# Kernel tuning notes

Hardware: AMD Instinct MI355X
Metric: run time of the kernel (lower is better)

The kernel has to match this reference:

```python
import jax, jax.numpy as jnp
import numpy as np

N_QUBITS = 14
N_TROTTER = 10
EVO_TIME = 1.0
BATCH = 2048
DIM = 2 ** N_QUBITS

# (-1)**bit_q(idx) for every basis index (Qiskit little-endian: qubit q <-> bit q)
_bits = (np.arange(DIM)[:, None] >> np.arange(N_QUBITS)[None, :]) & 1
_SIGNS = np.asarray(1 - 2 * _bits, dtype=np.float32)  # (DIM, n)


def _apply_1q(psi, U, q, n):
    A = 2 ** (n - 1 - q)
    B = 2 ** q
    psi = psi.reshape(A, 2, B)
    psi = jnp.einsum('ij,ajb->aib', U, psi)
    return psi.reshape(-1)


def _apply_zz(psi, theta, q, n):
    # CX(q,q+1); RZ(theta) on q+1; CX(q,q+1)  ==  diagonal exp(-i*theta/2 * Z_q Z_{q+1})
    A = 2 ** (n - 2 - q)
    B = 2 ** q
    em = jnp.exp(-0.5j * theta)
    ep = jnp.exp(0.5j * theta)
    diag = jnp.stack([em, ep, ep, em])  # axis index = 2*bit_{q+1} + bit_q
    psi = psi.reshape(A, 4, B) * diag[None, :, None]
    return psi.reshape(-1)


def _base_state(J, g):
    # Fixed part of the circuit (same for every sample): H on all qubits, then Trotter steps.
    n = N_QUBITS
    dt = EVO_TIME / N_TROTTER
    inv = 1.0 / np.sqrt(2.0)
    H = jnp.array([[inv, inv], [inv, -inv]], dtype=jnp.complex64)
    psi = jnp.zeros(DIM, dtype=jnp.complex64).at[0].set(1.0)
    for q in range(n):
        psi = _apply_1q(psi, H, q, n)
    for _ in range(N_TROTTER):
        for i in range(n - 1):
            psi = _apply_zz(psi, J[i] * dt, i, n)
        for i in range(n):
            half = 0.5 * g[i] * dt
            c = jnp.cos(half).astype(jnp.complex64)
            ms = -1j * jnp.sin(half)
            RX = jnp.stack([jnp.stack([c, ms]), jnp.stack([ms, c])])
            psi = _apply_1q(psi, RX, i, n)
    return psi


def _expectations(psi):
    # psi: (batch, DIM). Original observable order: block i -> qubit n-1-i, [X, Y, Z].
    n = N_QUBITS
    outs = []
    for i in range(n):
        q = n - 1 - i
        A = 2 ** (n - 1 - q)
        B = 2 ** q
        pr = psi.reshape(-1, A, 2, B)
        p0 = pr[:, :, 0, :]
        p1 = pr[:, :, 1, :]
        c = jnp.sum(jnp.conj(p0) * p1, axis=(1, 2))
        outs.append(2.0 * jnp.real(c))  # <X_q>
        outs.append(2.0 * jnp.imag(c))  # <Y_q>
        outs.append(jnp.sum(p0.real ** 2 + p0.imag ** 2 - p1.real ** 2 - p1.imag ** 2, axis=(1, 2)))  # <Z_q>
    return jnp.stack(outs, axis=1).astype(jnp.float32)


def setup_inputs() -> dict:
    key = jax.random.key(0)
    kx, kj, kg = jax.random.split(key, 3)
    x = jax.random.normal(kx, (BATCH, N_QUBITS), dtype=jnp.float32)
    J = jax.random.uniform(kj, (N_QUBITS - 1,), minval=0.5, maxval=1.5, dtype=jnp.float32)
    g = jax.random.uniform(kg, (N_QUBITS,), minval=0.5, maxval=1.5, dtype=jnp.float32)
    return {"x": x, "J": J, "g": g}


def reference(x, J, g):
    psi0 = _base_state(J, g)  # (DIM,), shared across the batch
    S = jnp.asarray(_SIGNS)   # (DIM, n)
    # Final per-sample RZ(x[b,q]) on qubit q -> diagonal phase exp(-i/2 * sum_q x_q * (-1)^bit_q)
    phase = jnp.exp((-0.5j) * (x @ S.T).astype(jnp.complex64))  # (batch, DIM)
    psi = psi0[None, :] * phase
    return _expectations(psi)
```

## Files before the change

kernel.cpp:

```cpp
#include <hip/hip_runtime.h>

#define NQ     14
#define DIMQ   16384
#define NTROT  10
#define NWG    16
#define NTHR   256

typedef float vfloat4 __attribute__((ext_vector_type(4)));

struct Smem {
    float2 slab[1024];
    float2 tabLo[64];
    float2 tabHi[128];
    float  red[48];
};

__device__ __forceinline__ float2 d2f2(double d) { union { double d; float2 f; } u; u.d = d; return u.f; }
__device__ __forceinline__ double f22d(float2 f) { union { double d; float2 f; } u; u.f = f; return u.d; }

__device__ __forceinline__ void ld4c(const float2* p, float2 r[4]) {
    vfloat4 a, b;
    asm volatile("global_load_dwordx4 %0, %2, off sc0 sc1\n\t"
                 "global_load_dwordx4 %1, %2, off offset:16 sc0 sc1\n\t"
                 "s_waitcnt vmcnt(0)"
                 : "=&v"(a), "=&v"(b) : "v"(p) : "memory");
    r[0] = make_float2(a.x, a.y); r[1] = make_float2(a.z, a.w);
    r[2] = make_float2(b.x, b.y); r[3] = make_float2(b.z, b.w);
}
__device__ __forceinline__ void st4c(float2* p, const float2 r[4]) {
    vfloat4 a, b;
    a.x = r[0].x; a.y = r[0].y; a.z = r[1].x; a.w = r[1].y;
    b.x = r[2].x; b.y = r[2].y; b.z = r[3].x; b.w = r[3].y;
    asm volatile("global_store_dwordx4 %0, %1, off sc0 sc1\n\t"
                 "global_store_dwordx4 %0, %2, off offset:16 sc0 sc1"
                 : : "v"(p), "v"(a), "v"(b) : "memory");
}
__device__ __forceinline__ void st2(float2* p, float2 v) {
    asm volatile("global_store_dwordx2 %0, %1, off sc0 sc1"
                 : : "v"(p), "v"(f22d(v)) : "memory");
}
__device__ __forceinline__ void stf(float* p, float v) {
    asm volatile("global_store_dword %0, %1, off sc0 sc1" : : "v"(p), "v"(v) : "memory");
}
__device__ __forceinline__ float ldf(const float* p) {
    float v;
    asm volatile("global_load_dword %0, %1, off sc0 sc1\n\ts_waitcnt vmcnt(0)"
                 : "=&v"(v) : "v"(p) : "memory");
    return v;
}
__device__ __forceinline__ void sti(int* p, int v) {
    asm volatile("global_store_dword %0, %1, off sc0 sc1" : : "v"(p), "v"(v) : "memory");
}
__device__ __forceinline__ int ldi(const int* p) {
    int v;
    asm volatile("global_load_dword %0, %1, off sc0 sc1\n\ts_waitcnt vmcnt(0)"
                 : "=&v"(v) : "v"(p) : "memory");
    return v;
}

__device__ __forceinline__ void gbar(int* flags, int w, int phase) {
    asm volatile("s_waitcnt vmcnt(0)" ::: "memory");
    __syncthreads();
    if (threadIdx.x < 64) {
        if (threadIdx.x == 0) sti(&flags[w], phase);
        for (;;) {
            int v = phase;
            if (threadIdx.x < NWG) v = ldi(&flags[threadIdx.x]);
            if (__ballot(v >= phase) == ~0ull) break;
            __builtin_amdgcn_s_sleep(1);
        }
    }
    __syncthreads();
}

__device__ __forceinline__ float2 cmulf(float2 a, float2 b) {
    return make_float2(a.x * b.x - a.y * b.y, a.x * b.y + a.y * b.x);
}
__device__ __forceinline__ void bfly(float2& p0, float2& p1, float c, float s) {
    float2 n0 = make_float2(c * p0.x + s * p1.y, c * p0.y - s * p1.x);
    float2 n1 = make_float2(c * p1.x + s * p0.y, c * p1.y - s * p0.x);
    p0 = n0; p1 = n1;
}
__device__ __forceinline__ void bfly_shfl(float2& p, int mask, float c, float s) {
    float qx = __shfl_xor(p.x, mask);
    float qy = __shfl_xor(p.y, mask);
    p = make_float2(c * p.x + s * qy, c * p.y - s * qx);
}
__device__ __forceinline__ void zz_apply(const Smem& sm, float2& a, int k) {
    int d = (k ^ (k >> 1)) & 0x1FFF;
    float2 rot = cmulf(sm.tabLo[d & 63], sm.tabHi[d >> 6]);
    a = cmulf(a, rot);
}
__device__ __forceinline__ void stage_12(float2* slab, float2 r[4], int t) {
    __syncthreads();
#pragma unroll
    for (int j = 0; j < 4; ++j) slab[(t << 2) | j] = r[j];
    __syncthreads();
#pragma unroll
    for (int j = 0; j < 4; ++j) r[j] = slab[t | (j << 8)];
}
__device__ __forceinline__ void stage_21(float2* slab, float2 r[4], int t) {
    __syncthreads();
#pragma unroll
    for (int j = 0; j < 4; ++j) slab[t | (j << 8)] = r[j];
    __syncthreads();
#pragma unroll
    for (int j = 0; j < 4; ++j) r[j] = slab[(t << 2) | j];
}
__device__ __forceinline__ void reduce_qubit(Smem& sm, int sb, int i, int t) {
    float cr = 0.f, ci = 0.f, z = 0.f;
#pragma unroll
    for (int j = 0; j < 4; ++j) {
        const int m = (t << 2) | j;
        const float2 a = sm.slab[m];
        const float n = a.x * a.x + a.y * a.y;
        if ((m >> sb) & 1) {
            z -= n;
        } else {
            z += n;
            const float2 b = sm.slab[m ^ (1 << sb)];
            cr += a.x * b.x + a.y * b.y;
            ci += a.x * b.y - a.y * b.x;
        }
    }
#pragma unroll
    for (int off = 32; off; off >>= 1) {
        cr += __shfl_down(cr, off);
        ci += __shfl_down(ci, off);
        z  += __shfl_down(z, off);
    }
    if ((t & 63) == 0) {
        atomicAdd(&sm.red[3 * i + 0], cr);
        atomicAdd(&sm.red[3 * i + 1], ci);
        atomicAdd(&sm.red[3 * i + 2], z);
    }
}

template <bool FIRST>
__device__ void phaseA(Smem& sm, float2* psi, int w, int t,
                       const float* c, const float* s) {
    float2 r[4];
    if (FIRST) {
#pragma unroll
        for (int j = 0; j < 4; ++j) r[j] = make_float2(0.0078125f, 0.0f);
    } else {
        ld4c(&psi[(w << 10) | (t << 2)], r);
#pragma unroll
        for (int b = 2; b < 6; ++b) {
#pragma unroll
            for (int j = 0; j < 4; ++j) bfly_shfl(r[j], 1 << b, c[2 + b], s[2 + b]);
        }
    }
#pragma unroll
    for (int j = 0; j < 4; ++j) zz_apply(sm, r[j], (w << 10) | (t << 2) | j);
    bfly(r[0], r[1], c[0], s[0]); bfly(r[2], r[3], c[0], s[0]);
    bfly(r[0], r[2], c[1], s[1]); bfly(r[1], r[3], c[1], s[1]);
#pragma unroll
    for (int b = 0; b < 6; ++b) {
#pragma unroll
        for (int j = 0; j < 4; ++j) bfly_shfl(r[j], 1 << b, c[2 + b], s[2 + b]);
    }
    stage_12(sm.slab, r, t);
    bfly(r[0], r[1], c[8], s[8]); bfly(r[2], r[3], c[8], s[8]);
    bfly(r[0], r[2], c[9], s[9]); bfly(r[1], r[3], c[9], s[9]);
#pragma unroll
    for (int j = 0; j < 4; ++j) st2(&psi[(w << 10) | t | (j << 8)], r[j]);
}

template <bool REDUCE>
__device__ void phaseB(Smem& sm, float2* psi, int w, int t,
                       const float* c, const float* s) {
    float2 r[4];
    const int kbase = ((t >> 2) << 8) | (w << 4) | ((t & 3) << 2);
    ld4c(&psi[kbase], r);
#pragma unroll
    for (int j = 0; j < 4; ++j) bfly_shfl(r[j], 16, c[10], s[10]);
#pragma unroll
    for (int j = 0; j < 4; ++j) bfly_shfl(r[j], 32, c[11], s[11]);
    stage_12(sm.slab, r, t);
    bfly(r[0], r[1], c[12], s[12]); bfly(r[2], r[3], c[12], s[12]);
    bfly(r[0], r[2], c[13], s[13]); bfly(r[1], r[3], c[13], s[13]);
#pragma unroll
    for (int j = 0; j < 4; ++j) {
        const int m = t | (j << 8);
        zz_apply(sm, r[j], ((m >> 4) << 8) | (w << 4) | (m & 15));
    }
    bfly(r[0], r[1], c[12], s[12]); bfly(r[2], r[3], c[12], s[12]);
    bfly(r[0], r[2], c[13], s[13]); bfly(r[1], r[3], c[13], s[13]);
#pragma unroll
    for (int b = 0; b < 4; ++b) {
#pragma unroll
        for (int j = 0; j < 4; ++j) bfly_shfl(r[j], 1 << b, c[b], s[b]);
    }
#pragma unroll
    for (int j = 0; j < 4; ++j) bfly_shfl(r[j], 16, c[8], s[8]);
#pragma unroll
    for (int j = 0; j < 4; ++j) bfly_shfl(r[j], 32, c[9], s[9]);
    stage_21(sm.slab, r, t);
#pragma unroll
    for (int j = 0; j < 4; ++j) bfly_shfl(r[j], 16, c[10], s[10]);
#pragma unroll
    for (int j = 0; j < 4; ++j) bfly_shfl(r[j], 32, c[11], s[11]);
    st4c(&psi[kbase], r);

    if (REDUCE) {
#pragma unroll
        for (int j = 0; j < 4; ++j) sm.slab[(t << 2) | j] = r[j];
        __syncthreads();
#pragma unroll
        for (int q = 0; q <= 3; ++q) reduce_qubit(sm, q, 13 - q, t);
#pragma unroll
        for (int q = 8; q <= 13; ++q) reduce_qubit(sm, q - 4, 13 - q, t);
    }
}

__device__ void phaseA_final(Smem& sm, const float2* psi, int w, int t,
                             const float* c, const float* s, float* P) {
    float2 r[4];
    ld4c(&psi[(w << 10) | (t << 2)], r);
#pragma unroll
    for (int b = 2; b < 6; ++b) {
#pragma unroll
        for (int j = 0; j < 4; ++j) bfly_shfl(r[j], 1 << b, c[2 + b], s[2 + b]);
    }
    __syncthreads();
#pragma unroll
    for (int j = 0; j < 4; ++j) sm.slab[(t << 2) | j] = r[j];
    __syncthreads();
#pragma unroll
    for (int q = 4; q <= 7; ++q) reduce_qubit(sm, q, 13 - q, t);
    __syncthreads();
    if (t < 42) stf(&P[t * NWG + w], sm.red[t]);
}

extern "C" __global__ void __launch_bounds__(NTHR)
qr_all(const float* __restrict__ x, const float* __restrict__ J,
       const float* __restrict__ g, float* __restrict__ out,
       float2* __restrict__ psi, float* __restrict__ P,
       int* __restrict__ flags) {
    __shared__ Smem sm;
    const int w = blockIdx.x;
    const int t = threadIdx.x;
    const float dt = 0.1f;

    if (t < 64) {
        float phi = 0.0f;
        for (int i = 0; i < 6; ++i) {
            const float h = 0.5f * J[i] * dt;
            phi += ((t >> i) & 1) ? h : -h;
        }
        float sn, cs; __sincosf(phi, &sn, &cs);
        sm.tabLo[t] = make_float2(cs, sn);
    } else if (t < 192) {
        const int v = t - 64;
        float phi = 0.0f;
        for (int i = 0; i < 7; ++i) {
            const float h = 0.5f * J[6 + i] * dt;
            phi += ((v >> i) & 1) ? h : -h;
        }
        float sn, cs; __sincosf(phi, &sn, &cs);
        sm.tabHi[v] = make_float2(cs, sn);
    }
    if (t < 48) sm.red[t] = 0.0f;
    float cc[NQ], ss[NQ];
#pragma unroll
    for (int i = 0; i < NQ; ++i) __sincosf(0.5f * g[i] * dt, &ss[i], &cc[i]);
    __syncthreads();

    int bar = 0;
    phaseA<true>(sm, psi, w, t, cc, ss);
    gbar(flags, w, ++bar);
    for (int sstep = 1; sstep <= 9; ++sstep) {
        if (sstep & 1) {
            if (sstep == 9) phaseB<true >(sm, psi, w, t, cc, ss);
            else            phaseB<false>(sm, psi, w, t, cc, ss);
        } else {
            phaseA<false>(sm, psi, w, t, cc, ss);
        }
        gbar(flags, w, ++bar);
    }
    phaseA_final(sm, psi, w, t, cc, ss, P);
    gbar(flags, w, ++bar);

    float* sumbuf = (float*)sm.slab;
    for (int idx = t; idx < 42 * NWG; idx += NTHR) sumbuf[idx] = ldf(&P[idx]);
    __syncthreads();
    float cv = 0.0f;
    if (t < 42) {
#pragma unroll
        for (int k = 0; k < NWG; ++k) cv += sumbuf[t * NWG + k];
    }
    __syncthreads();
    if (t < 42) sm.red[t] = cv;
    __syncthreads();

    for (int task = w * NTHR + t; task < 2048 * NQ; task += NWG * NTHR) {
        const int b = task / NQ;
        const int i = task - b * NQ;
        const int q = 13 - i;
        const float xv = x[b * NQ + q];
        const float cr = sm.red[3 * i + 0];
        const float ci = sm.red[3 * i + 1];
        const float zz = sm.red[3 * i + 2];
        float sn, cs; __sincosf(xv, &sn, &cs);
        float* o = out + b * (3 * NQ) + 3 * i;
        o[0] = 2.0f * (cs * cr - sn * ci);
        o[1] = 2.0f * (sn * cr + cs * ci);
        o[2] = zz;
    }
}

extern "C" void kernel_launch(void* const* d_in, const int* in_sizes, int n_in,
                              void* d_out, int out_size, void* d_ws, size_t ws_size,
                              hipStream_t stream) {
    const float* x = (const float*)d_in[0];
    const float* J = (const float*)d_in[1];
    const float* g = (const float*)d_in[2];
    float* out = (float*)d_out;
    char* ws   = (char*)d_ws;
    float2* psi  = (float2*)ws;
    int*    flags = (int*)(ws + DIMQ * sizeof(float2));
    float*  P     = (float*)(ws + DIMQ * sizeof(float2) + 256);
    (void)in_sizes; (void)n_in; (void)out_size; (void)ws_size;

    hipLaunchKernelGGL(qr_all, dim3(NWG), dim3(NTHR), 0, stream,
                       x, J, g, out, psi, P, flags);
}
```

Measured before the change: 106.3 us.

## Use per-wave split arrive/wait grid barrier and overlap work with barrier waits

Replaces the workgroup-level grid barrier, which needed two __syncthreads and a single polling wave, with per-wavefront arrive flags (64 waves) polled by every wave without sleeping. Arrive and wait are split so independent work runs in between: the sincos of the x inputs for the output stage is computed while waiting on the first barrier, and the final-step qubit reductions are done before waiting. This removes intra-block syncs from each of the ten barriers. In exchange, all waves busy-spin on global loads, which adds memory traffic, and seven extra sincos values stay live in registers across the loop.

After: 125.3 us. 17.9% more time.

```diff
diff --git a/kernel.cpp b/kernel.cpp
--- a/kernel.cpp
+++ b/kernel.cpp
@@ -5,6 +5,7 @@
 #define NTROT  10
 #define NWG    16
 #define NTHR   256
+#define NWAVE  64
 
 typedef float vfloat4 __attribute__((ext_vector_type(4)));
 
@@ -58,19 +59,16 @@
     return v;
 }
 
-__device__ __forceinline__ void gbar(int* flags, int w, int phase) {
+__device__ __forceinline__ void arrive(int* wf, int wid, int phase) {
     asm volatile("s_waitcnt vmcnt(0)" ::: "memory");
-    __syncthreads();
-    if (threadIdx.x < 64) {
-        if (threadIdx.x == 0) sti(&flags[w], phase);
-        for (;;) {
-            int v = phase;
-            if (threadIdx.x < NWG) v = ldi(&flags[threadIdx.x]);
-            if (__ballot(v >= phase) == ~0ull) break;
-            __builtin_amdgcn_s_sleep(1);
-        }
-    }
-    __syncthreads();
+    if ((threadIdx.x & 63) == 0) sti(&wf[wid], phase);
+}
+__device__ __forceinline__ void waitbar(const int* wf, int phase) {
+    const int lane = threadIdx.x & 63;
+    for (;;) {
+        int v = ldi(&wf[lane]);
+        if (__ballot(v >= phase) == ~0ull) break;
+    }
 }
 
 __device__ __forceinline__ float2 cmulf(float2 a, float2 b) {
@@ -167,7 +165,7 @@
     for (int j = 0; j < 4; ++j) st2(&psi[(w << 10) | t | (j << 8)], r[j]);
 }
 
-template <bool REDUCE>
+template <bool KEEPSLAB>
 __device__ void phaseB(Smem& sm, float2* psi, int w, int t,
                        const float* c, const float* s) {
     float2 r[4];
@@ -202,45 +200,21 @@
 #pragma unroll
     for (int j = 0; j < 4; ++j) bfly_shfl(r[j], 32, c[11], s[11]);
     st4c(&psi[kbase], r);
-
-    if (REDUCE) {
+    if (KEEPSLAB) {
 #pragma unroll
         for (int j = 0; j < 4; ++j) sm.slab[(t << 2) | j] = r[j];
-        __syncthreads();
-#pragma unroll
-        for (int q = 0; q <= 3; ++q) reduce_qubit(sm, q, 13 - q, t);
-#pragma unroll
-        for (int q = 8; q <= 13; ++q) reduce_qubit(sm, q - 4, 13 - q, t);
-    }
-}
-
-__device__ void phaseA_final(Smem& sm, const float2* psi, int w, int t,
-                             const float* c, const float* s, float* P) {
-    float2 r[4];
-    ld4c(&psi[(w << 10) | (t << 2)], r);
-#pragma unroll
-    for (int b = 2; b < 6; ++b) {
-#pragma unroll
-        for (int j = 0; j < 4; ++j) bfly_shfl(r[j], 1 << b, c[2 + b], s[2 + b]);
-    }
-    __syncthreads();
-#pragma unroll
-    for (int j = 0; j < 4; ++j) sm.slab[(t << 2) | j] = r[j];
-    __syncthreads();
-#pragma unroll
-    for (int q = 4; q <= 7; ++q) reduce_qubit(sm, q, 13 - q, t);
-    __syncthreads();
-    if (t < 42) stf(&P[t * NWG + w], sm.red[t]);
+    }
 }
 
 extern "C" __global__ void __launch_bounds__(NTHR)
 qr_all(const float* __restrict__ x, const float* __restrict__ J,
        const float* __restrict__ g, float* __restrict__ out,
        float2* __restrict__ psi, float* __restrict__ P,
-       int* __restrict__ flags) {
+       int* __restrict__ wf) {
     __shared__ Smem sm;
     const int w = blockIdx.x;
     const int t = threadIdx.x;
+    const int wid = (w << 2) | (t >> 6);
     const float dt = 0.1f;
 
     if (t < 64) {
@@ -269,18 +243,59 @@
 
     int bar = 0;
     phaseA<true>(sm, psi, w, t, cc, ss);
-    gbar(flags, w, ++bar);
+    arrive(wf, wid, ++bar);
+    float esn[7], ecs[7];
+#pragma unroll
+    for (int k = 0; k < 7; ++k) {
+        const int task = w * NTHR + t + (k << 12);
+        const int b = task / NQ;
+        const int i = task - b * NQ;
+        __sincosf(x[b * NQ + 13 - i], &esn[k], &ecs[k]);
+    }
+    waitbar(wf, bar);
+
     for (int sstep = 1; sstep <= 9; ++sstep) {
         if (sstep & 1) {
-            if (sstep == 9) phaseB<true >(sm, psi, w, t, cc, ss);
-            else            phaseB<false>(sm, psi, w, t, cc, ss);
+            if (sstep == 9) {
+                phaseB<true>(sm, psi, w, t, cc, ss);
+                arrive(wf, wid, ++bar);
+                __syncthreads();
+#pragma unroll
+                for (int q = 0; q <= 3; ++q) reduce_qubit(sm, q, 13 - q, t);
+#pragma unroll
+                for (int q = 8; q <= 13; ++q) reduce_qubit(sm, q - 4, 13 - q, t);
+                waitbar(wf, bar);
+            } else {
+                phaseB<false>(sm, psi, w, t, cc, ss);
+                arrive(wf, wid, ++bar);
+                waitbar(wf, bar);
+            }
         } else {
             phaseA<false>(sm, psi, w, t, cc, ss);
-        }
-        gbar(flags, w, ++bar);
-    }
-    phaseA_final(sm, psi, w, t, cc, ss, P);
-    gbar(flags, w, ++bar);
+            arrive(wf, wid, ++bar);
+            waitbar(wf, bar);
+        }
+    }
+
+    {
+        float2 r[4];
+        ld4c(&psi[(w << 10) | (t << 2)], r);
+#pragma unroll
+        for (int b = 2; b < 6; ++b) {
+#pragma unroll
+            for (int j = 0; j < 4; ++j) bfly_shfl(r[j], 1 << b, cc[2 + b], ss[2 + b]);
+        }
+        __syncthreads();
+#pragma unroll
+        for (int j = 0; j < 4; ++j) sm.slab[(t << 2) | j] = r[j];
+        __syncthreads();
+#pragma unroll
+        for (int q = 4; q <= 7; ++q) reduce_qubit(sm, q, 13 - q, t);
+        __syncthreads();
+        if (t < 42) stf(&P[t * NWG + w], sm.red[t]);
+        arrive(wf, wid, ++bar);
+        waitbar(wf, bar);
+    }
 
     float* sumbuf = (float*)sm.slab;
     for (int idx = t; idx < 42 * NWG; idx += NTHR) sumbuf[idx] = ldf(&P[idx]);
@@ -294,15 +309,15 @@
     if (t < 42) sm.red[t] = cv;
     __syncthreads();
 
-    for (int task = w * NTHR + t; task < 2048 * NQ; task += NWG * NTHR) {
+#pragma unroll
+    for (int k = 0; k < 7; ++k) {
+        const int task = w * NTHR + t + (k << 12);
         const int b = task / NQ;
         const int i = task - b * NQ;
-        const int q = 13 - i;
-        const float xv = x[b * NQ + q];
         const float cr = sm.red[3 * i + 0];
         const float ci = sm.red[3 * i + 1];
         const float zz = sm.red[3 * i + 2];
-        float sn, cs; __sincosf(xv, &sn, &cs);
+        const float sn = esn[k], cs = ecs[k];
         float* o = out + b * (3 * NQ) + 3 * i;
         o[0] = 2.0f * (cs * cr - sn * ci);
         o[1] = 2.0f * (sn * cr + cs * ci);
@@ -318,11 +333,11 @@
     const float* g = (const float*)d_in[2];
     float* out = (float*)d_out;
     char* ws   = (char*)d_ws;
-    float2* psi  = (float2*)ws;
-    int*    flags = (int*)(ws + DIMQ * sizeof(float2));
-    float*  P     = (float*)(ws + DIMQ * sizeof(float2) + 256);
+    float2* psi = (float2*)ws;
+    int*    wf  = (int*)(ws + DIMQ * sizeof(float2));
+    float*  P   = (float*)(ws + DIMQ * sizeof(float2) + 256);
     (void)in_sizes; (void)n_in; (void)out_size; (void)ws_size;
 
     hipLaunchKernelGGL(qr_all, dim3(NWG), dim3(NTHR), 0, stream,
-                       x, J, g, out, psi, P, flags);
-}
+                       x, J, g, out, psi, P, wf);
+}
```
